# Kernel tuning notes

Measured on AMD Instinct MI355X. Metric: run time of the kernel, lower is better.

The kernel has to match this reference:

```python
import jax, jax.numpy as jnp
import numpy as np

EPS = 1e-08
SPARSITY = 0.1  # fraction of (node, hyperedge) incidences set to 1


def setup_inputs() -> dict:
    key = jax.random.key(0)
    k_x, k_w, k_h, k_W, k_b = jax.random.split(key, 5)
    B, N, E, Din, Dout = 8, 4096, 2048, 256, 256
    x = jax.random.normal(k_x, (B, N, Din), dtype=jnp.float32)
    edge_weight = jax.random.uniform(k_w, (E,), dtype=jnp.float32)
    H = (jax.random.uniform(k_h, (N, E)) < SPARSITY).astype(jnp.float32)
    # nn.Linear params
    bound = 1.0 / np.sqrt(Din)
    W = jax.random.uniform(k_W, (Dout, Din), minval=-bound, maxval=bound, dtype=jnp.float32)
    b = jax.random.uniform(k_b, (Dout,), minval=-bound, maxval=bound, dtype=jnp.float32)
    return {"x": x, "edge_weight": edge_weight, "H": H, "W": W, "b": b}


def _build_adjacency(H, edge_weight):
    # dv = H @ diag(w) @ 1 = H @ w ; de = H.sum(0)
    dv = H @ edge_weight                      # [N]
    de = H.sum(axis=0)                        # [E]
    dv_is = jnp.power(dv + EPS, -0.5)         # Dv^{-1/2} diagonal
    de_inv = jnp.power(de + EPS, -1.0)        # De^{-1} diagonal
    # A = Dv^{-1/2} H W De^{-1} H^T Dv^{-1/2}; apply diagonals as row/col scales
    Hw = H * (edge_weight * de_inv)[None, :]  # [N, E]
    A = (dv_is[:, None] * (Hw @ H.T)) * dv_is[None, :]  # [N, N]
    return A


def reference(x, edge_weight, H, W, b):
    A = _build_adjacency(H, edge_weight)
    xw = jnp.einsum('bnd,od->bno', x, W) + b  # Linear: [B, N, Dout]
    out = jnp.einsum('ij,bjd->bid', A, xw)    # hypergraph propagation
    return out
```

## Files before the change

### kernel.cpp

```cpp
#include <hip/hip_runtime.h>
#include <hip/hip_bf16.h>

typedef __hip_bfloat16 bf16;
typedef __bf16 bfx8 __attribute__((ext_vector_type(8)));
typedef float f32x4 __attribute__((ext_vector_type(4)));

typedef __attribute__((address_space(3))) void lds_void_t;
typedef const __attribute__((address_space(1))) void gbl_void_t;

__global__ void prep_kernel(const float* __restrict__ H, const float* __restrict__ w,
                            bf16* __restrict__ HT, bf16* __restrict__ Hb,
                            float* __restrict__ de, float* __restrict__ dvr, int N, int E) {
    __shared__ bf16 tile[64][65];
    __shared__ float cred[4][64];
    __shared__ float rred[4][64];
    int eb = blockIdx.x * 64, nb = blockIdx.y * 64;
    int tid = threadIdx.x;
    int c = tid & 63, g = tid >> 6;

    float cs = 0.f;
#pragma unroll
    for (int k = 0; k < 16; k++) {
        int r = g + (k << 2);
        float v = H[(size_t)(nb + r) * E + eb + c];
        bf16 bv = __float2bfloat16(v);
        tile[r][c] = bv;
        if (Hb) Hb[(size_t)(nb + r) * E + eb + c] = bv;
        cs += v;
    }
    cred[g][c] = cs;
    __syncthreads();
    if (g == 0) {
        float s = cred[0][c] + cred[1][c] + cred[2][c] + cred[3][c];
        atomicAdd(&de[eb + c], s);
    }
    float rs = 0.f;
#pragma unroll
    for (int k = 0; k < 16; k++) {
        int cc = g + (k << 2);
        rs += __bfloat162float(tile[c][cc]) * w[eb + cc];
    }
    rred[g][c] = rs;
    __syncthreads();
    if (g == 1) {
        float s = rred[0][c] + rred[1][c] + rred[2][c] + rred[3][c];
        atomicAdd(&dvr[nb + c], s);
    }
#pragma unroll
    for (int k = 0; k < 16; k++) {
        int r = g + (k << 2);
        HT[(size_t)(eb + r) * N + nb + c] = tile[c][r];
    }
}

__global__ __launch_bounds__(256) void gemm_k3(
    const float* __restrict__ W, const float* __restrict__ x,
    const float* __restrict__ bias, const float* __restrict__ dvr,
    bf16* __restrict__ xs_t) {
    __shared__ __align__(16) bf16 As[256 * 40];
    __shared__ __align__(16) bf16 Bs[64 * 40];

    const int bx = blockIdx.x, z = blockIdx.y;
    const int tid = threadIdx.x;
    const int wave = tid >> 6, lane = tid & 63;
    const int wr = wave * 64;
    const int lcol = lane & 15, quad = lane >> 4;
    const float* xp = x + (size_t)z * 1048576 + (size_t)bx * 64 * 256;

    f32x4 acc[4][4];
#pragma unroll
    for (int i = 0; i < 4; i++)
#pragma unroll
        for (int j = 0; j < 4; j++) acc[i][j] = (f32x4){0.f, 0.f, 0.f, 0.f};

    for (int k0 = 0; k0 < 256; k0 += 32) {
#pragma unroll
        for (int c = 0; c < 4; c++) {
            int ch = tid + c * 256;
            int r = ch >> 2, kc = (ch & 3) << 3;
            f32x4 p0 = *(const f32x4*)&W[(size_t)r * 256 + k0 + kc];
            f32x4 p1 = *(const f32x4*)&W[(size_t)r * 256 + k0 + kc + 4];
            bfx8 va;
#pragma unroll
            for (int t = 0; t < 4; t++) { va[t] = (__bf16)p0[t]; va[4 + t] = (__bf16)p1[t]; }
            *(bfx8*)&As[r * 40 + kc] = va;
        }
        {
            int r = tid >> 2, kc = (tid & 3) << 3;
            f32x4 q0 = *(const f32x4*)&xp[(size_t)r * 256 + k0 + kc];
            f32x4 q1 = *(const f32x4*)&xp[(size_t)r * 256 + k0 + kc + 4];
            bfx8 vb;
#pragma unroll
            for (int t = 0; t < 4; t++) { vb[t] = (__bf16)q0[t]; vb[4 + t] = (__bf16)q1[t]; }
            *(bfx8*)&Bs[r * 40 + kc] = vb;
        }
        __syncthreads();

        bfx8 af[4], bfr[4];
#pragma unroll
        for (int i = 0; i < 4; i++)
            af[i] = *(const bfx8*)&As[(wr + i * 16 + lcol) * 40 + quad * 8];
#pragma unroll
        for (int j = 0; j < 4; j++)
            bfr[j] = *(const bfx8*)&Bs[(j * 16 + lcol) * 40 + quad * 8];
#pragma unroll
        for (int i = 0; i < 4; i++)
#pragma unroll
            for (int j = 0; j < 4; j++)
                acc[i][j] = __builtin_amdgcn_mfma_f32_16x16x32_bf16(af[i], bfr[j], acc[i][j], 0, 0, 0);
        __syncthreads();
    }

#pragma unroll
    for (int j = 0; j < 4; j++) {
        int n = bx * 64 + j * 16 + lcol;
        float dn = rsqrtf(dvr[n] + 1e-8f);
#pragma unroll
        for (int i = 0; i < 4; i++) {
#pragma unroll
            for (int r = 0; r < 4; r++) {
                int o = wr + i * 16 + quad * 4 + r;
                float v = (acc[i][j][r] + bias[o]) * dn;
                xs_t[(size_t)(z * 256 + o) * 4096 + n] = __float2bfloat16(v);
            }
        }
    }
}


#define STG_A(cb, h, u) do { \
    __builtin_amdgcn_global_load_lds((gbl_void_t*)(ga##h##0 + (size_t)(u) * 64), \
        (lds_void_t*)&SM[(cb) * 16384 + (h) * 8192 + dOff], 16, 0, 0); \
    __builtin_amdgcn_global_load_lds((gbl_void_t*)(ga##h##1 + (size_t)(u) * 64), \
        (lds_void_t*)&SM[(cb) * 16384 + (h) * 8192 + 4096 + dOff], 16, 0, 0); \
} while (0)

#define STG_B(cb, h, u) do { \
    __builtin_amdgcn_global_load_lds((gbl_void_t*)(gb##h##0 + (size_t)(u) * 64), \
        (lds_void_t*)&SM[32768 + (cb) * 16384 + (h) * 8192 + dOff], 16, 0, 0); \
    __builtin_amdgcn_global_load_lds((gbl_void_t*)(gb##h##1 + (size_t)(u) * 64), \
        (lds_void_t*)&SM[32768 + (cb) * 16384 + (h) * 8192 + 4096 + dOff], 16, 0, 0); \
} while (0)

#define LDA_(cb, qi, i, kk) \
    (*(const bfx8*)&SM[(cb) * 16384 + aBase + ((qi) * 64 + (i) * 16) * 64 + ra##kk])
#define LDB_(cb, j, kk) \
    (*(const bfx8*)&SM[32768 + (cb) * 16384 + bjb[j] + ra##kk])

#define PH_MFMA(I0, J0) do { \
    __builtin_amdgcn_s_setprio(1); \
    _Pragma("unroll") \
    for (int i_ = 0; i_ < 4; i_++) { \
        _Pragma("unroll") \
        for (int jj_ = 0; jj_ < 2; jj_++) { \
            acc[(I0) + i_][(J0) + jj_] = __builtin_amdgcn_mfma_f32_16x16x32_bf16( \
                af[i_][0], bf[(J0) + jj_][0], acc[(I0) + i_][(J0) + jj_], 0, 0, 0); \
            acc[(I0) + i_][(J0) + jj_] = __builtin_amdgcn_mfma_f32_16x16x32_bf16( \
                af[i_][1], bf[(J0) + jj_][1], acc[(I0) + i_][(J0) + jj_], 0, 0, 0); \
        } \
    } \
    __builtin_amdgcn_s_setprio(0); \
} while (0)

#define KTILE(cb, uA, uB) do { \
     \
    _Pragma("unroll") \
    for (int i_ = 0; i_ < 4; i_++) { af[i_][0] = LDA_(cb, 0, i_, 0); af[i_][1] = LDA_(cb, 0, i_, 1); } \
    _Pragma("unroll") \
    for (int j_ = 0; j_ < 2; j_++) { bf[j_][0] = LDB_(cb, j_, 0); bf[j_][1] = LDB_(cb, j_, 1); } \
    STG_A((cb) ^ 1, 0, uA); \
    STG_A((cb) ^ 1, 1, uA); \
    __builtin_amdgcn_s_barrier(); \
    PH_MFMA(0, 0); \
    __builtin_amdgcn_s_barrier(); \
     \
    _Pragma("unroll") \
    for (int j_ = 0; j_ < 2; j_++) { bf[2 + j_][0] = LDB_(cb, 2 + j_, 0); bf[2 + j_][1] = LDB_(cb, 2 + j_, 1); } \
    __builtin_amdgcn_s_barrier(); \
    PH_MFMA(0, 2); \
    __builtin_amdgcn_s_barrier(); \
     \
    _Pragma("unroll") \
    for (int i_ = 0; i_ < 4; i_++) { af[i_][0] = LDA_(cb, 1, i_, 0); af[i_][1] = LDA_(cb, 1, i_, 1); } \
    STG_B(cb, 0, uB); \
    __builtin_amdgcn_s_barrier(); \
    PH_MFMA(4, 2); \
    __builtin_amdgcn_s_barrier(); \
     \
    STG_B(cb, 1, uB); \
    __builtin_amdgcn_s_barrier(); \
    PH_MFMA(4, 0); \
    asm volatile("s_waitcnt vmcnt(4)" ::: "memory"); \
    __builtin_amdgcn_s_barrier(); \
} while (0)

__global__ __launch_bounds__(512, 2) void gemm8ph(
    const bf16* __restrict__ A, const bf16* __restrict__ Bt, int Kst, int kLen,
    bf16* __restrict__ S0, bf16* __restrict__ S1, bf16* __restrict__ S2, bf16* __restrict__ S3,
    int ldc) {
    __shared__ __align__(16) bf16 SM[65536];

    const int nx = gridDim.x, ny = gridDim.y;
    const int nwg = nx * ny * gridDim.z;
    const int lin = (blockIdx.z * ny + blockIdx.y) * nx + blockIdx.x;
    const int cpx = nwg >> 3;
    const int swz = (lin & 7) * cpx + (lin >> 3);
    const int bx = swz % nx;
    const int t1 = swz / nx;
    const int by = t1 % ny;
    const int bz = t1 / ny;
    bf16* Cs = (bz == 0) ? S0 : (bz == 1) ? S1 : (bz == 2) ? S2 : S3;
    const int kBase = bz * kLen;
    const int NT = kLen >> 6;

    const int tid = threadIdx.x;
    const int lane = tid & 63, wave = tid >> 6;
    const int lcol = lane & 15, quad = lane >> 4;
    const int wr = (wave >> 2) * 128, wc = (wave & 3) * 64;
    const int aBase = (wave >> 2) * 8192;
    const int xr = lcol & 7;

    const int rowBase = by * 256, colBase = bx * 256;

    const int ra0 = lcol * 64 + ((quad ^ xr) << 3);
    const int ra1 = lcol * 64 + (((4 + quad) ^ xr) << 3);
    int bjb[4];
#pragma unroll
    for (int j = 0; j < 4; j++) {
        int rg = wc + j * 16;
        bjb[j] = ((rg >> 7) * 8192) + ((rg & 127) * 64);
    }

    const int srow = tid >> 3, slot = tid & 7;
    const int r0 = srow, r1 = srow + 64;
    const int sx0 = (slot ^ (r0 & 7)) << 3;
    const int sx1 = (slot ^ (r1 & 7)) << 3;
    const bf16* ga00 = A + (size_t)(rowBase + r0) * Kst + kBase + sx0;
    const bf16* ga01 = A + (size_t)(rowBase + r1) * Kst + kBase + sx1;
    const bf16* ga10 = A + (size_t)(rowBase + 128 + r0) * Kst + kBase + sx0;
    const bf16* ga11 = A + (size_t)(rowBase + 128 + r1) * Kst + kBase + sx1;
    const bf16* gb00 = Bt + (size_t)(colBase + r0) * Kst + kBase + sx0;
    const bf16* gb01 = Bt + (size_t)(colBase + r1) * Kst + kBase + sx1;
    const bf16* gb10 = Bt + (size_t)(colBase + 128 + r0) * Kst + kBase + sx0;
    const bf16* gb11 = Bt + (size_t)(colBase + 128 + r1) * Kst + kBase + sx1;
    const int dOff = tid * 8;

    f32x4 acc[8][4];
#pragma unroll
    for (int i = 0; i < 8; i++)
#pragma unroll
        for (int j = 0; j < 4; j++) acc[i][j] = (f32x4){0.f, 0.f, 0.f, 0.f};
    bfx8 af[4][2], bf[4][2];

    STG_A(0, 0, 0); STG_A(0, 1, 0); STG_B(0, 0, 0); STG_B(0, 1, 0);
    STG_B(1, 0, 1); STG_B(1, 1, 1);
    asm volatile("s_waitcnt vmcnt(4)" ::: "memory");
    __builtin_amdgcn_s_barrier();

    const int nPairs = NT >> 1;
    for (int it = 0; it < nPairs; ++it) {
        int u1 = 2 * it + 1;
        int u2 = 2 * it + 2; if (u2 > NT - 1) u2 = NT - 1;
        int u3 = 2 * it + 3; if (u3 > NT - 1) u3 = NT - 1;
        KTILE(0, u1, u2);
        KTILE(1, u2, u3);
    }

#pragma unroll
    for (int i = 0; i < 8; i++) {
#pragma unroll
        for (int j = 0; j < 4; j++) {
#pragma unroll
            for (int r = 0; r < 4; r++) {
                int grow = rowBase + wr + i * 16 + quad * 4 + r;
                int gcol = colBase + wc + j * 16 + lcol;
                Cs[(size_t)grow * ldc + gcol] = __float2bfloat16(acc[i][j][r]);
            }
        }
    }
}

__global__ void combine4_kernel(const bf16* __restrict__ s0, const bf16* __restrict__ s1,
                                const bf16* __restrict__ s2, const bf16* __restrict__ s3,
                                const float* __restrict__ w, const float* __restrict__ de,
                                bf16* __restrict__ tt) {
    size_t i = ((size_t)blockIdx.x * 256 + threadIdx.x) * 8;
    int e = (int)(i & 2047);
    bfx8 a = *(const bfx8*)&s0[i];
    bfx8 b = *(const bfx8*)&s1[i];
    bfx8 c = *(const bfx8*)&s2[i];
    bfx8 d = *(const bfx8*)&s3[i];
    bfx8 v;
#pragma unroll
    for (int t = 0; t < 8; t++) {
        float ws = w[e + t] / (de[e + t] + 1e-8f);
        v[t] = (__bf16)((((float)a[t] + (float)b[t]) + ((float)c[t] + (float)d[t])) * ws);
    }
    *(bfx8*)&tt[i] = v;
}

__global__ void transpose_kernel(const bf16* __restrict__ src, bf16* __restrict__ dst,
                                 int R, int C) {
    __shared__ __bf16 t[64][68];
    int cb = blockIdx.x * 64, rb = blockIdx.y * 64;
    int tid = threadIdx.x;
    int lc = tid & 7, lr = tid >> 3;
#pragma unroll
    for (int p = 0; p < 2; p++) {
        int r = lr + p * 32;
        bfx8 v = *(const bfx8*)&src[(size_t)(rb + r) * C + cb + lc * 8];
#pragma unroll
        for (int q = 0; q < 8; q++) t[r][lc * 8 + q] = v[q];
    }
    __syncthreads();
#pragma unroll
    for (int p = 0; p < 2; p++) {
        int c = lr + p * 32;
        bfx8 v;
#pragma unroll
        for (int q = 0; q < 8; q++) v[q] = t[lc * 8 + q][c];
        *(bfx8*)&dst[(size_t)(cb + c) * R + rb + lc * 8] = v;
    }
}

__global__ void combine_out_kernel(const bf16* __restrict__ sA, const bf16* __restrict__ sB,
                                   const float* __restrict__ dvr, float* __restrict__ out) {
    size_t t8 = ((size_t)blockIdx.x * 256 + threadIdx.x) * 8;
    int o = (int)(t8 & 255);
    int n = (int)((t8 >> 8) & 4095);
    int b = (int)(t8 >> 20);
    size_t si = (size_t)n * 2048 + b * 256 + o;
    bfx8 a = *(const bfx8*)&sA[si];
    bfx8 bb = *(const bfx8*)&sB[si];
    float d = rsqrtf(dvr[n] + 1e-8f);
    f32x4 v0, v1;
#pragma unroll
    for (int t = 0; t < 4; t++) {
        v0[t] = d * ((float)a[t] + (float)bb[t]);
        v1[t] = d * ((float)a[4 + t] + (float)bb[4 + t]);
    }
    *(f32x4*)&out[t8] = v0;
    *(f32x4*)&out[t8 + 4] = v1;
}

extern "C" void kernel_launch(void* const* d_in, const int* in_sizes, int n_in,
                              void* d_out, int out_size, void* d_ws, size_t ws_size,
                              hipStream_t stream) {
    const float* x    = (const float*)d_in[0];
    const float* ew   = (const float*)d_in[1];
    const float* H    = (const float*)d_in[2];
    const float* W    = (const float*)d_in[3];
    const float* bias = (const float*)d_in[4];

    const int N = 4096, E = 2048;

    char* ws = (char*)d_ws;
    float* de   = (float*)(ws);
    float* dvr  = (float*)(ws + 8192);
    bf16*  HT   = (bf16*)(ws + 65536);
    bf16*  xs_t = (bf16*)(ws + 65536 + 16777216);
    bf16*  t_t  = (bf16*)(ws + 65536 + 33554432);
    bf16*  wsHb = (bf16*)(ws + 65536 + 41943040);
    const bool bigws = ws_size >= 58785792ull + 4096ull;

    bf16* s0 = (bf16*)d_out;
    bf16* s1 = s0 + 4194304;
    bf16* s2 = s0 + 2 * 4194304;
    bf16* s3 = s0 + 3 * 4194304;
    bf16* k5a = HT;
    bf16* k5b = xs_t;

    (void)hipMemsetAsync(ws, 0, 24576, stream);

    prep_kernel<<<dim3(E / 64, N / 64), 256, 0, stream>>>(
        H, ew, HT, bigws ? wsHb : nullptr, de, dvr, N, E);

    gemm_k3<<<dim3(64, 8), 256, 0, stream>>>(W, x, bias, dvr, xs_t);

    gemm8ph<<<dim3(8, 8, 4), 512, 0, stream>>>(xs_t, HT, 4096, 1024, s0, s1, s2, s3, 2048);

    combine4_kernel<<<dim3(2048), 256, 0, stream>>>(s0, s1, s2, s3, ew, de, t_t);

    bf16* HbP = bigws ? wsHb : (bf16*)d_out;
    if (!bigws) {
        transpose_kernel<<<dim3(64, 32), 256, 0, stream>>>(HT, HbP, 2048, 4096);
    }

    gemm8ph<<<dim3(8, 16, 2), 512, 0, stream>>>(HbP, t_t, 2048, 1024, k5a, k5b, k5a, k5a, 2048);

    combine_out_kernel<<<dim3(4096), 256, 0, stream>>>(k5a, k5b, dvr, (float*)d_out);
}
```

Measured before the change: 219.9 us.

## Fuse split-K reductions into GEMM epilogue via last-arriving-block atomic flags

Each split-K GEMM block increments a per-tile atomic counter after writing its partial, and the last block to arrive sums all partials and applies the scaling (edge-weight/degree for the first GEMM, Dv^-1/2 with fp32 output for the second). This removes the separate combine4 and combine_out launches and their extra global round trip. It also moves the second half of the A-tile staging later in the k-loop to spread out global loads. The cost is threadfences, atomics and a serialized epilogue done by one block per tile.

```diff
diff --git a/kernel.cpp b/kernel.cpp
--- a/kernel.cpp
+++ b/kernel.cpp
@@ -169,13 +169,13 @@
     _Pragma("unroll") \
     for (int j_ = 0; j_ < 2; j_++) { bf[j_][0] = LDB_(cb, j_, 0); bf[j_][1] = LDB_(cb, j_, 1); } \
     STG_A((cb) ^ 1, 0, uA); \
-    STG_A((cb) ^ 1, 1, uA); \
     __builtin_amdgcn_s_barrier(); \
     PH_MFMA(0, 0); \
     __builtin_amdgcn_s_barrier(); \
      \
     _Pragma("unroll") \
     for (int j_ = 0; j_ < 2; j_++) { bf[2 + j_][0] = LDB_(cb, 2 + j_, 0); bf[2 + j_][1] = LDB_(cb, 2 + j_, 1); } \
+    STG_A((cb) ^ 1, 1, uA); \
     __builtin_amdgcn_s_barrier(); \
     PH_MFMA(0, 2); \
     __builtin_amdgcn_s_barrier(); \
@@ -194,10 +194,12 @@
     __builtin_amdgcn_s_barrier(); \
 } while (0)
 
+template <int MODE>
 __global__ __launch_bounds__(512, 2) void gemm8ph(
     const bf16* __restrict__ A, const bf16* __restrict__ Bt, int Kst, int kLen,
-    bf16* __restrict__ S0, bf16* __restrict__ S1, bf16* __restrict__ S2, bf16* __restrict__ S3,
-    int ldc) {
+    bf16* __restrict__ P, long long sStride, int ldc,
+    int* __restrict__ flags, const float* __restrict__ sv1, const float* __restrict__ sv2,
+    bf16* __restrict__ ttOut, float* __restrict__ outF) {
     __shared__ __align__(16) bf16 SM[65536];
 
     const int nx = gridDim.x, ny = gridDim.y;
@@ -209,9 +211,9 @@
     const int t1 = swz / nx;
     const int by = t1 % ny;
     const int bz = t1 / ny;
-    bf16* Cs = (bz == 0) ? S0 : (bz == 1) ? S1 : (bz == 2) ? S2 : S3;
     const int kBase = bz * kLen;
     const int NT = kLen >> 6;
+    const int NZ = (MODE == 4) ? 4 : 2;
 
     const int tid = threadIdx.x;
     const int lane = tid & 63, wave = tid >> 6;
@@ -266,6 +268,7 @@
         KTILE(1, u2, u3);
     }
 
+    bf16* Ps = P + (size_t)bz * (size_t)sStride;
 #pragma unroll
     for (int i = 0; i < 8; i++) {
 #pragma unroll
@@ -274,29 +277,63 @@
             for (int r = 0; r < 4; r++) {
                 int grow = rowBase + wr + i * 16 + quad * 4 + r;
                 int gcol = colBase + wc + j * 16 + lcol;
-                Cs[(size_t)grow * ldc + gcol] = __float2bfloat16(acc[i][j][r]);
+                Ps[(size_t)grow * ldc + gcol] = __float2bfloat16(acc[i][j][r]);
             }
         }
     }
-}
-
-__global__ void combine4_kernel(const bf16* __restrict__ s0, const bf16* __restrict__ s1,
-                                const bf16* __restrict__ s2, const bf16* __restrict__ s3,
-                                const float* __restrict__ w, const float* __restrict__ de,
-                                bf16* __restrict__ tt) {
-    size_t i = ((size_t)blockIdx.x * 256 + threadIdx.x) * 8;
-    int e = (int)(i & 2047);
-    bfx8 a = *(const bfx8*)&s0[i];
-    bfx8 b = *(const bfx8*)&s1[i];
-    bfx8 c = *(const bfx8*)&s2[i];
-    bfx8 d = *(const bfx8*)&s3[i];
-    bfx8 v;
-#pragma unroll
-    for (int t = 0; t < 8; t++) {
-        float ws = w[e + t] / (de[e + t] + 1e-8f);
-        v[t] = (__bf16)((((float)a[t] + (float)b[t]) + ((float)c[t] + (float)d[t])) * ws);
-    }
-    *(bfx8*)&tt[i] = v;
+    if (flags == nullptr) return;
+
+    __threadfence();
+    int* lastP = (int*)&SM[4096];
+    if (tid == 0) lastP[0] = (atomicAdd(&flags[by * nx + bx], 1) == NZ - 1) ? 1 : 0;
+    __syncthreads();
+    if (lastP[0] == 0) return;
+    __threadfence();
+
+    if (MODE == 4) {
+        float* wscL = (float*)&SM[0];
+        if (tid < 256) {
+            int e = colBase + tid;
+            wscL[tid] = sv1[e] / (sv2[e] + 1e-8f);
+        }
+        __syncthreads();
+#pragma unroll 4
+        for (int rep = 0; rep < 16; rep++) {
+            int idx = rep * 512 + tid;
+            int row = idx >> 5, ch = idx & 31;
+            size_t off = (size_t)(rowBase + row) * ldc + colBase + ch * 8;
+            bfx8 p0 = *(const bfx8*)&P[off];
+            bfx8 p1 = *(const bfx8*)&P[(size_t)sStride + off];
+            bfx8 p2 = *(const bfx8*)&P[2 * (size_t)sStride + off];
+            bfx8 p3 = *(const bfx8*)&P[3 * (size_t)sStride + off];
+            bfx8 o;
+#pragma unroll
+            for (int q = 0; q < 8; q++)
+                o[q] = (__bf16)((((float)p0[q] + (float)p1[q]) + ((float)p2[q] + (float)p3[q])) *
+                                wscL[ch * 8 + q]);
+            *(bfx8*)&ttOut[off] = o;
+        }
+    } else {
+#pragma unroll 4
+        for (int rep = 0; rep < 16; rep++) {
+            int idx = rep * 512 + tid;
+            int row = idx >> 5, ch = idx & 31;
+            int n = rowBase + row;
+            float dv = rsqrtf(sv1[n] + 1e-8f);
+            size_t poff = (size_t)n * ldc + colBase + ch * 8;
+            bfx8 a = *(const bfx8*)&P[poff];
+            bfx8 b2 = *(const bfx8*)&P[(size_t)sStride + poff];
+            size_t ooff = (size_t)(colBase >> 8) * 1048576 + (size_t)n * 256 + ch * 8;
+            f32x4 w0, w1;
+#pragma unroll
+            for (int t = 0; t < 4; t++) {
+                w0[t] = dv * ((float)a[t] + (float)b2[t]);
+                w1[t] = dv * ((float)a[4 + t] + (float)b2[4 + t]);
+            }
+            *(f32x4*)&outF[ooff] = w0;
+            *(f32x4*)&outF[ooff + 4] = w1;
+        }
+    }
 }
 
 __global__ void transpose_kernel(const bf16* __restrict__ src, bf16* __restrict__ dst,
@@ -326,9 +363,9 @@
 __global__ void combine_out_kernel(const bf16* __restrict__ sA, const bf16* __restrict__ sB,
                                    const float* __restrict__ dvr, float* __restrict__ out) {
     size_t t8 = ((size_t)blockIdx.x * 256 + threadIdx.x) * 8;
-    int o = (int)(t8 & 255);
     int n = (int)((t8 >> 8) & 4095);
     int b = (int)(t8 >> 20);
+    int o = (int)(t8 & 255);
     size_t si = (size_t)n * 2048 + b * 256 + o;
     bfx8 a = *(const bfx8*)&sA[si];
     bfx8 bb = *(const bfx8*)&sB[si];
@@ -355,8 +392,10 @@
     const int N = 4096, E = 2048;
 
     char* ws = (char*)d_ws;
-    float* de   = (float*)(ws);
-    float* dvr  = (float*)(ws + 8192);
+    float* de     = (float*)(ws);
+    float* dvr    = (float*)(ws + 8192);
+    int*   flags4 = (int*)(ws + 24576);
+    int*   flags5 = (int*)(ws + 25088);
     bf16*  HT   = (bf16*)(ws + 65536);
     bf16*  xs_t = (bf16*)(ws + 65536 + 16777216);
     bf16*  t_t  = (bf16*)(ws + 65536 + 33554432);
@@ -364,29 +403,29 @@
     const bool bigws = ws_size >= 58785792ull + 4096ull;
 
     bf16* s0 = (bf16*)d_out;
-    bf16* s1 = s0 + 4194304;
-    bf16* s2 = s0 + 2 * 4194304;
-    bf16* s3 = s0 + 3 * 4194304;
     bf16* k5a = HT;
     bf16* k5b = xs_t;
 
-    (void)hipMemsetAsync(ws, 0, 24576, stream);
+    (void)hipMemsetAsync(ws, 0, 25600, stream);
 
     prep_kernel<<<dim3(E / 64, N / 64), 256, 0, stream>>>(
         H, ew, HT, bigws ? wsHb : nullptr, de, dvr, N, E);
 
     gemm_k3<<<dim3(64, 8), 256, 0, stream>>>(W, x, bias, dvr, xs_t);
 
-    gemm8ph<<<dim3(8, 8, 4), 512, 0, stream>>>(xs_t, HT, 4096, 1024, s0, s1, s2, s3, 2048);
-
-    combine4_kernel<<<dim3(2048), 256, 0, stream>>>(s0, s1, s2, s3, ew, de, t_t);
+    gemm8ph<4><<<dim3(8, 8, 4), 512, 0, stream>>>(
+        xs_t, HT, 4096, 1024, s0, 4194304LL, 2048, flags4, ew, de, t_t, nullptr);
 
     bf16* HbP = bigws ? wsHb : (bf16*)d_out;
     if (!bigws) {
         transpose_kernel<<<dim3(64, 32), 256, 0, stream>>>(HT, HbP, 2048, 4096);
     }
 
-    gemm8ph<<<dim3(8, 16, 2), 512, 0, stream>>>(HbP, t_t, 2048, 1024, k5a, k5b, k5a, k5a, 2048);
-
-    combine_out_kernel<<<dim3(4096), 256, 0, stream>>>(k5a, k5b, dvr, (float*)d_out);
-}
+    gemm8ph<5><<<dim3(8, 16, 2), 512, 0, stream>>>(
+        HbP, t_t, 2048, 1024, k5a, 8388608LL, 2048,
+        bigws ? flags5 : nullptr, dvr, nullptr, nullptr, (float*)d_out);
+
+    if (!bigws) {
+        combine_out_kernel<<<dim3(4096), 256, 0, stream>>>(k5a, k5b, dvr, (float*)d_out);
+    }
+}
```

Measured after the change: 424.7 us. 93.1% more time.
